# Kernel optimization log

Measured on AMD Instinct MI355X. Metric: run time of the kernel, lower is better.

The kernel has to match this reference:

```python
import jax, jax.numpy as jnp
import numpy as np

N = 32768
NIN = 12
NC = 16
HID = 512
K = 8
B = 3.0
L = 8
D_HALF = NIN // 2                      # 6
DIN = D_HALF + NC                      # conditioner input
DOUT = (3 * K - 1) * (NIN - D_HALF)    # conditioner output
MIN_W = 1e-3
MIN_H = 1e-3
MIN_D = 1e-3
DERIV_CONST = float(np.log(np.exp(1.0 - MIN_D) - 1.0))  # softplus^{-1}(1-min_d)


def setup_inputs() -> dict:
    key = jax.random.key(0)
    ks = jax.random.split(key, 12)
    z = jax.random.normal(ks[0], (N, NIN), dtype=jnp.float32)
    c = jax.random.normal(ks[1], (N, NC), dtype=jnp.float32)

    def lin(k, fan_in, shape):
        bound = 1.0 / np.sqrt(fan_in)
        return jax.random.uniform(k, shape, jnp.float32, -bound, bound)

    W0 = lin(ks[2], DIN, (L, DIN, HID)); b0 = lin(ks[3], DIN, (L, HID))
    W1 = lin(ks[4], HID, (L, HID, HID)); b1 = lin(ks[5], HID, (L, HID))
    W2 = lin(ks[6], HID, (L, HID, HID)); b2 = lin(ks[7], HID, (L, HID))
    W3 = lin(ks[8], HID, (L, HID, DOUT)); b3 = lin(ks[9], HID, (L, DOUT))

    rng = np.random.default_rng(0)
    perms = jnp.asarray(np.stack([rng.permutation(NIN) for _ in range(L - 1)]),
                        dtype=jnp.int32)  # [L-1, NIN]
    return dict(z=z, c=c, W0=W0, b0=b0, W1=W1, b1=b1, W2=W2, b2=b2,
                W3=W3, b3=b3, perms=perms)


def _rqs(x, uw, uh, ud):
    """Unconstrained rational-quadratic spline (forward).
    x: [N, d2]; uw/uh: [N, d2, K]; ud: [N, d2, K+1] (already edge-padded)."""
    widths = jax.nn.softmax(uw, axis=-1)
    widths = MIN_W + (1.0 - MIN_W * K) * widths
    cw = jnp.cumsum(widths, axis=-1)
    cw = jnp.concatenate([jnp.zeros_like(cw[..., :1]), cw], axis=-1)
    cw = 2.0 * B * cw - B
    cw = cw.at[..., 0].set(-B).at[..., -1].set(B)
    w = cw[..., 1:] - cw[..., :-1]

    heights = jax.nn.softmax(uh, axis=-1)
    heights = MIN_H + (1.0 - MIN_H * K) * heights
    ch = jnp.cumsum(heights, axis=-1)
    ch = jnp.concatenate([jnp.zeros_like(ch[..., :1]), ch], axis=-1)
    ch = 2.0 * B * ch - B
    ch = ch.at[..., 0].set(-B).at[..., -1].set(B)
    h = ch[..., 1:] - ch[..., :-1]

    d = MIN_D + jax.nn.softplus(ud)  # [N, d2, K+1]

    xc = jnp.clip(x, -B, B)  # tails are handled by mask below
    # searchsorted: eps added only to the last knot for the search itself
    cw_search = cw.at[..., -1].add(1e-6)
    idx = jnp.clip(jnp.sum((xc[..., None] >= cw_search).astype(jnp.int32),
                           axis=-1) - 1, 0, K - 1)  # [N, d2]

    def g(a):
        return jnp.take_along_axis(a, idx[..., None], axis=-1)[..., 0]

    icw, iw = g(cw), g(w)
    ich, ih = g(ch), g(h)
    idelta = g(h / w)
    id0 = g(d)
    id1 = g(d[..., 1:])

    theta = (xc - icw) / iw
    t1m = theta * (1.0 - theta)
    num = ih * (idelta * theta**2 + id0 * t1m)
    den = idelta + (id0 + id1 - 2.0 * idelta) * t1m
    out = ich + num / den
    dnum = idelta**2 * (id1 * theta**2 + 2.0 * idelta * t1m
                        + id0 * (1.0 - theta)**2)
    lad = jnp.log(dnum) - 2.0 * jnp.log(den)

    inside = (x >= -B) & (x <= B)
    return jnp.where(inside, out, x), jnp.where(inside, lad, 0.0)


def _flow(z, c, W0, b0, W1, b1, W2, b2, W3, b3, perms):
    x = z
    total_ld = jnp.zeros(z.shape[0], dtype=z.dtype)
    for i in range(L):
        x1, x2 = x[:, :D_HALF], x[:, D_HALF:]
        inp = jnp.concatenate([x1, c], axis=-1)
        h0 = jax.nn.elu(inp @ W0[i] + b0[i])
        h1 = jax.nn.elu(h0 @ W1[i] + b1[i])
        h2 = jax.nn.elu(h1 @ W2[i] + b2[i])
        out = (h2 @ W3[i] + b3[i]).reshape(-1, NIN - D_HALF, 3 * K - 1)
        uw, uh, ud = out[..., :K], out[..., K:2 * K], out[..., 2 * K:]
        ud = jnp.pad(ud, ((0, 0), (0, 0), (1, 1)),
                     constant_values=DERIV_CONST)
        x2n, ld = _rqs(x2, uw, uh, ud)
        total_ld = total_ld + jnp.sum(ld, axis=-1)
        x = jnp.concatenate([x1, x2n], axis=-1)
        if i < L - 1:
            x = x[:, perms[i]]
    return x, total_ld


def reference(z, c, W0, b0, W1, b1, W2, b2, W3, b3, perms):
    return _flow(z, c, W0, b0, W1, b1, W2, b2, W3, b3, perms)
```

## Files before the change

### kernel.cpp

```cpp
#include <hip/hip_runtime.h>
#include <hip/hip_fp16.h>

#define NROWS   32768
#define MT      64
#define NTH     512
#define HS      520
#define OS      148
#define BND     3.0f

typedef _Float16 half_t;
typedef __attribute__((ext_vector_type(8))) _Float16 f16x8;
typedef __attribute__((ext_vector_type(4))) _Float16 f16x4;
typedef __attribute__((ext_vector_type(4))) float    f32x4;


__global__ void pack_frag(const float* __restrict__ src, half_t* __restrict__ dst,
                          int K, int Nn, int NT, int KS) {
  int l = blockIdx.z;
  int frag = blockIdx.x * 4 + (threadIdx.x >> 6);
  int lane = threadIdx.x & 63;
  int NF = NT * KS;
  if (frag >= NF) return;
  int nt = frag / KS, ks = frag - nt * KS;
  int n = nt * 16 + (lane & 15);
  int kb = ks * 32 + (lane >> 4) * 8;
  f16x8 v;
#pragma unroll
  for (int e = 0; e < 8; e++) {
    int k = kb + e;
    v[e] = (k < K && n < Nn) ? (half_t)src[((size_t)l * K + k) * Nn + n] : (half_t)0.f;
  }
  *(f16x8*)(dst + ((size_t)l * NF + frag) * 512 + lane * 8) = v;
}

__device__ __forceinline__ float elu_f(float v) {
  return v > 0.f ? v : (__expf(v) - 1.f);
}

__device__ __forceinline__ void gemm_elu(
    const half_t* A, int as, int ksteps,
    const half_t* __restrict__ Wf, int KSW,
    const float* __restrict__ bias,
    half_t* dst,
    int w, int lane, int lm, int lk) {
  f16x8 a[2][4], b[4][2];
#pragma unroll
  for (int half = 0; half < 2; half++) {
    const int ntb = w * 4 + half * 2;
    f32x4 acc[4][2];
#pragma unroll
    for (int i = 0; i < 4; i++)
#pragma unroll
      for (int j = 0; j < 2; j++) acc[i][j] = (f32x4){0.f, 0.f, 0.f, 0.f};

    const bool prefilled = (ksteps == 16) && (half == 1);
    if (!prefilled) {
#pragma unroll
      for (int s = 0; s < 4; s++)
        if (s < ksteps) {
#pragma unroll
          for (int nt = 0; nt < 2; nt++)
            b[s][nt] = *(const f16x8*)(Wf + ((size_t)((ntb + nt) * KSW + s)) * 512 + lane * 8);
        }
#pragma unroll
      for (int s = 0; s < 2; s++)
        if (s < ksteps) {
          int ko = s * 32 + lk * 8;
#pragma unroll
          for (int mf = 0; mf < 4; mf++)
            a[s][mf] = *(const f16x8*)(A + (mf * 16 + lm) * as + ko);
        }
    }
#pragma unroll
    for (int ks = 0; ks < ksteps; ks++) {
      const int sl = ks & 3, asx = ks & 1;
#pragma unroll
      for (int nt = 0; nt < 2; nt++)
#pragma unroll
        for (int mf = 0; mf < 4; mf++)
          acc[mf][nt] = __builtin_amdgcn_mfma_f32_16x16x32_f16(b[sl][nt], a[asx][mf], acc[mf][nt], 0, 0, 0);
      if (ks + 4 < ksteps) {
#pragma unroll
        for (int nt = 0; nt < 2; nt++)
          b[sl][nt] = *(const f16x8*)(Wf + ((size_t)((ntb + nt) * KSW + ks + 4)) * 512 + lane * 8);
      } else if (ksteps == 16 && half == 0) {
#pragma unroll
        for (int nt = 0; nt < 2; nt++)
          b[sl][nt] = *(const f16x8*)(Wf + ((size_t)((ntb + 2 + nt) * KSW + (ks - 12))) * 512 + lane * 8);
      }
      if (ks + 2 < ksteps) {
        int ko = (ks + 2) * 32 + lk * 8;
#pragma unroll
        for (int mf = 0; mf < 4; mf++)
          a[asx][mf] = *(const f16x8*)(A + (mf * 16 + lm) * HS + ko);
      } else if (ksteps == 16 && half == 0) {
        int ko = (ks - 14) * 32 + lk * 8;
#pragma unroll
        for (int mf = 0; mf < 4; mf++)
          a[asx][mf] = *(const f16x8*)(A + (mf * 16 + lm) * HS + ko);
      }
    }
#pragma unroll
    for (int nt = 0; nt < 2; nt++) {
      int n0 = w * 64 + half * 32 + nt * 16 + lk * 4;
      f32x4 bv = *(const f32x4*)(bias + n0);
#pragma unroll
      for (int mf = 0; mf < 4; mf++) {
        f16x4 pv;
#pragma unroll
        for (int r = 0; r < 4; r++) pv[r] = (half_t)elu_f(acc[mf][nt][r] + bv[r]);
        *(f16x4*)(dst + (mf * 16 + lm) * HS + n0) = pv;
      }
    }
  }
}

__device__ __forceinline__ void gemm_out(
    const half_t* A,
    const half_t* __restrict__ Wf,
    const float* __restrict__ bias,
    float* outb,
    int w, int lane, int lm, int lk) {
  f32x4 acc[4][2];
#pragma unroll
  for (int i = 0; i < 4; i++)
#pragma unroll
    for (int j = 0; j < 2; j++) acc[i][j] = (f32x4){0.f, 0.f, 0.f, 0.f};
  const bool has2 = (w == 0);

  f16x8 a[2][4], b[4][2];
#pragma unroll
  for (int s = 0; s < 4; s++) {
    b[s][0] = *(const f16x8*)(Wf + ((size_t)(w * 16 + s)) * 512 + lane * 8);
    if (has2) b[s][1] = *(const f16x8*)(Wf + ((size_t)(8 * 16 + s)) * 512 + lane * 8);
  }
#pragma unroll
  for (int s = 0; s < 2; s++) {
    int ko = s * 32 + lk * 8;
#pragma unroll
    for (int mf = 0; mf < 4; mf++)
      a[s][mf] = *(const f16x8*)(A + (mf * 16 + lm) * HS + ko);
  }
#pragma unroll
  for (int ks = 0; ks < 16; ks++) {
    const int sl = ks & 3, asx = ks & 1;
#pragma unroll
    for (int mf = 0; mf < 4; mf++)
      acc[mf][0] = __builtin_amdgcn_mfma_f32_16x16x32_f16(b[sl][0], a[asx][mf], acc[mf][0], 0, 0, 0);
    if (has2)
#pragma unroll
      for (int mf = 0; mf < 4; mf++)
        acc[mf][1] = __builtin_amdgcn_mfma_f32_16x16x32_f16(b[sl][1], a[asx][mf], acc[mf][1], 0, 0, 0);
    if (ks + 4 < 16) {
      b[sl][0] = *(const f16x8*)(Wf + ((size_t)(w * 16 + ks + 4)) * 512 + lane * 8);
      if (has2) b[sl][1] = *(const f16x8*)(Wf + ((size_t)(128 + ks + 4)) * 512 + lane * 8);
    }
    if (ks + 2 < 16) {
      int ko = (ks + 2) * 32 + lk * 8;
#pragma unroll
      for (int mf = 0; mf < 4; mf++)
        a[asx][mf] = *(const f16x8*)(A + (mf * 16 + lm) * HS + ko);
    }
  }
  {
    int n0 = w * 16 + lk * 4;
    f32x4 bv = *(const f32x4*)(bias + n0);
#pragma unroll
    for (int mf = 0; mf < 4; mf++) {
      f32x4 ov = acc[mf][0] + bv;
      *(f32x4*)(outb + (mf * 16 + lm) * OS + n0) = ov;
    }
  }
  if (has2) {
    int n0 = 128 + lk * 4;
    f32x4 bv;
#pragma unroll
    for (int r = 0; r < 4; r++) bv[r] = (n0 + r < 138) ? bias[n0 + r] : 0.f;
#pragma unroll
    for (int mf = 0; mf < 4; mf++) {
      f32x4 ov = acc[mf][1] + bv;
      *(f32x4*)(outb + (mf * 16 + lm) * OS + n0) = ov;
    }
  }
}

__global__ __launch_bounds__(NTH, 2) __attribute__((amdgpu_waves_per_eu(2, 2)))
void flow_kernel(const float* __restrict__ z, const float* __restrict__ c,
                 const float* __restrict__ b0, const float* __restrict__ b1,
                 const float* __restrict__ b2, const float* __restrict__ b3,
                 const int* __restrict__ perms,
                 const half_t* __restrict__ W0F, const half_t* __restrict__ W1F,
                 const half_t* __restrict__ W2F, const half_t* __restrict__ W3F,
                 float* __restrict__ out) {
  __shared__ half_t hbufA[MT * HS];
  __shared__ __align__(16) char smemB[MT * HS * 2];
  __shared__ half_t inpb[MT * 40];
  __shared__ half_t cbuf[MT * 16];
  __shared__ float xbuf[MT][12];
  __shared__ float ldpart[MT][6];
  __shared__ float ldtot[MT];
  __shared__ int   permbuf[7][12];

  half_t* hbufB  = (half_t*)smemB;
  float*  outbuf = (float*)smemB;

  int tid = threadIdx.x;
  int w = tid >> 6, lane = tid & 63;
  int lm = lane & 15, lk = lane >> 4;
  int row0 = blockIdx.x * MT;

  for (int it = tid; it < MT * 12; it += NTH) xbuf[it / 12][it % 12] = z[(size_t)row0 * 12 + it];
  for (int it = tid; it < MT * 16; it += NTH) cbuf[it] = (half_t)c[(size_t)row0 * 16 + it];
  for (int it = tid; it < 84; it += NTH) permbuf[it / 12][it % 12] = perms[it];
  if (tid < MT) ldtot[tid] = 0.f;
  __syncthreads();

  for (int l = 0; l < 8; l++) {
    for (int it = tid; it < MT * 32; it += NTH) {
      int m = it >> 5, k = it & 31;
      half_t bv;
      if (k < 6)       bv = (half_t)xbuf[m][k];
      else if (k < 22) bv = cbuf[m * 16 + (k - 6)];
      else             bv = (half_t)0.f;
      inpb[m * 40 + k] = bv;
    }
    __syncthreads();
    gemm_elu(inpb, 40, 1,  W0F + (size_t)l * 32 * 512,      1,  b0 + l * 512, hbufA, w, lane, lm, lk);
    __syncthreads();
    gemm_elu(hbufA, HS, 16, W1F + (size_t)l * 512 * 512,   16,  b1 + l * 512, hbufB, w, lane, lm, lk);
    __syncthreads();
    gemm_elu(hbufB, HS, 16, W2F + (size_t)l * 512 * 512,   16,  b2 + l * 512, hbufA, w, lane, lm, lk);
    __syncthreads();
    gemm_out(hbufA, W3F + (size_t)l * 144 * 512, b3 + l * 138, outbuf, w, lane, lm, lk);
    __syncthreads();

    if (tid < MT * 6) {
      int m = tid / 6, j = tid % 6;
      const float* pr = outbuf + m * OS + j * 23;
      float uw[8], uh[8], dd[9];
#pragma unroll
      for (int i = 0; i < 8; i++) uw[i] = pr[i];
#pragma unroll
      for (int i = 0; i < 8; i++) uh[i] = pr[8 + i];
      dd[0] = 1.f; dd[8] = 1.f;
#pragma unroll
      for (int i = 0; i < 7; i++) {
        float u = pr[16 + i];
        float sp = (u > 15.f) ? u : log1pf(__expf(u));
        dd[i + 1] = 0.001f + sp;
      }
      float mw = uw[0];
#pragma unroll
      for (int i = 1; i < 8; i++) mw = fmaxf(mw, uw[i]);
      float ew[8], sw = 0.f;
#pragma unroll
      for (int i = 0; i < 8; i++) { ew[i] = __expf(uw[i] - mw); sw += ew[i]; }
      float invw = 1.f / sw;
      float cw[9]; cw[0] = -BND;
      float a = 0.f;
#pragma unroll
      for (int i = 0; i < 8; i++) { a += 0.001f + 0.992f * ew[i] * invw; cw[i + 1] = 2.f * BND * a - BND; }
      cw[8] = BND;
      float mh = uh[0];
#pragma unroll
      for (int i = 1; i < 8; i++) mh = fmaxf(mh, uh[i]);
      float eh[8], sh = 0.f;
#pragma unroll
      for (int i = 0; i < 8; i++) { eh[i] = __expf(uh[i] - mh); sh += eh[i]; }
      float invh = 1.f / sh;
      float ch[9]; ch[0] = -BND;
      float ah = 0.f;
#pragma unroll
      for (int i = 0; i < 8; i++) { ah += 0.001f + 0.992f * eh[i] * invh; ch[i + 1] = 2.f * BND * ah - BND; }
      ch[8] = BND;

      float x2 = xbuf[m][6 + j];
      float xc = fminf(fmaxf(x2, -BND), BND);
      int cnt = 0;
#pragma unroll
      for (int i = 0; i < 9; i++) {
        float edge = (i == 8) ? (cw[8] + 1e-6f) : cw[i];
        cnt += (xc >= edge) ? 1 : 0;
      }
      int idx = cnt - 1; idx = idx < 0 ? 0 : (idx > 7 ? 7 : idx);
      float icw = cw[0], iw = cw[1] - cw[0], ich = ch[0], ih = ch[1] - ch[0], d0 = dd[0], d1 = dd[1];
#pragma unroll
      for (int i = 0; i < 8; i++) {
        if (idx == i) {
          icw = cw[i]; iw = cw[i + 1] - cw[i];
          ich = ch[i]; ih = ch[i + 1] - ch[i];
          d0 = dd[i]; d1 = dd[i + 1];
        }
      }
      float delta = ih / iw;
      float th  = (xc - icw) / iw;
      float t1m = th * (1.f - th);
      float num = ih * (delta * th * th + d0 * t1m);
      float den = delta + (d0 + d1 - 2.f * delta) * t1m;
      float outv = ich + num / den;
      float dnum = delta * delta * (d1 * th * th + 2.f * delta * t1m + d0 * (1.f - th) * (1.f - th));
      float lad = logf(dnum) - 2.f * logf(den);
      bool inside = (x2 >= -BND) && (x2 <= BND);
      xbuf[m][6 + j] = inside ? outv : x2;
      ldpart[m][j]   = inside ? lad : 0.f;
    }
    __syncthreads();
    if (tid < MT) {
      float s = ldtot[tid];
#pragma unroll
      for (int j = 0; j < 6; j++) s += ldpart[tid][j];
      ldtot[tid] = s;
    }
    if (l < 7) {
      float v0 = xbuf[tid / 12][permbuf[l][tid % 12]];
      float v1 = 0.f;
      int it1 = tid + NTH;
      if (it1 < MT * 12) v1 = xbuf[it1 / 12][permbuf[l][it1 % 12]];
      __syncthreads();
      xbuf[tid / 12][tid % 12] = v0;
      if (it1 < MT * 12) xbuf[it1 / 12][it1 % 12] = v1;
    }
    __syncthreads();
  }

  for (int it = tid; it < MT * 12; it += NTH) out[(size_t)row0 * 12 + it] = xbuf[it / 12][it % 12];
  if (tid < MT) out[(size_t)NROWS * 12 + row0 + tid] = ldtot[tid];
}

extern "C" void kernel_launch(void* const* d_in, const int* in_sizes, int n_in,
                              void* d_out, int out_size, void* d_ws, size_t ws_size,
                              hipStream_t stream) {
  const float* z  = (const float*)d_in[0];
  const float* c  = (const float*)d_in[1];
  const float* W0 = (const float*)d_in[2];
  const float* b0 = (const float*)d_in[3];
  const float* W1 = (const float*)d_in[4];
  const float* b1 = (const float*)d_in[5];
  const float* W2 = (const float*)d_in[6];
  const float* b2 = (const float*)d_in[7];
  const float* W3 = (const float*)d_in[8];
  const float* b3 = (const float*)d_in[9];
  const int* perms = (const int*)d_in[10];

  unsigned short* wsu = (unsigned short*)d_ws;
  half_t* W0F = (half_t*)(wsu + 0);
  half_t* W1F = (half_t*)(wsu + 131072);
  half_t* W2F = (half_t*)(wsu + 2228224);
  half_t* W3F = (half_t*)(wsu + 4325376);

  pack_frag<<<dim3(8,   1, 8), dim3(256), 0, stream>>>(W0, W0F, 22,  512, 32, 1);
  pack_frag<<<dim3(128, 1, 8), dim3(256), 0, stream>>>(W1, W1F, 512, 512, 32, 16);
  pack_frag<<<dim3(128, 1, 8), dim3(256), 0, stream>>>(W2, W2F, 512, 512, 32, 16);
  pack_frag<<<dim3(36,  1, 8), dim3(256), 0, stream>>>(W3, W3F, 512, 138, 9,  16);

  flow_kernel<<<dim3(NROWS / MT), dim3(NTH), 0, stream>>>(
      z, c, b0, b1, b2, b3, perms, W0F, W1F, W2F, W3F, (float*)d_out);
}
```

Measured before the change: 551.7 us.

## Store hidden activations in MFMA fragment-packed shared memory layout

Hidden activation buffers in shared memory are reorganized from padded row-major into the same per-lane fragment order used by the MFMA A operand, so each lane reads a contiguous 16-byte chunk indexed by lane. The ELU epilogue writes results directly into this packed order, and the input staging packs the first layer's operand similarly. This aims to reduce address arithmetic and LDS bank conflicts on operand reads and drops the row padding, at the cost of possibly less favorable store patterns in the epilogue.

```diff
diff --git a/kernel.cpp b/kernel.cpp
--- a/kernel.cpp
+++ b/kernel.cpp
@@ -4,7 +4,6 @@
 #define NROWS   32768
 #define MT      64
 #define NTH     512
-#define HS      520
 #define OS      148
 #define BND     3.0f
 
@@ -38,7 +37,7 @@
 }
 
 __device__ __forceinline__ void gemm_elu(
-    const half_t* A, int as, int ksteps,
+    const half_t* A, int KSA, int ksteps,
     const half_t* __restrict__ Wf, int KSW,
     const float* __restrict__ bias,
     half_t* dst,
@@ -65,10 +64,9 @@
 #pragma unroll
       for (int s = 0; s < 2; s++)
         if (s < ksteps) {
-          int ko = s * 32 + lk * 8;
 #pragma unroll
           for (int mf = 0; mf < 4; mf++)
-            a[s][mf] = *(const f16x8*)(A + (mf * 16 + lm) * as + ko);
+            a[s][mf] = *(const f16x8*)(A + ((size_t)(mf * KSA + s)) * 512 + lane * 8);
         }
     }
 #pragma unroll
@@ -89,27 +87,29 @@
           b[sl][nt] = *(const f16x8*)(Wf + ((size_t)((ntb + 2 + nt) * KSW + (ks - 12))) * 512 + lane * 8);
       }
       if (ks + 2 < ksteps) {
-        int ko = (ks + 2) * 32 + lk * 8;
 #pragma unroll
         for (int mf = 0; mf < 4; mf++)
-          a[asx][mf] = *(const f16x8*)(A + (mf * 16 + lm) * HS + ko);
+          a[asx][mf] = *(const f16x8*)(A + ((size_t)(mf * KSA + ks + 2)) * 512 + lane * 8);
       } else if (ksteps == 16 && half == 0) {
-        int ko = (ks - 14) * 32 + lk * 8;
 #pragma unroll
         for (int mf = 0; mf < 4; mf++)
-          a[asx][mf] = *(const f16x8*)(A + (mf * 16 + lm) * HS + ko);
-      }
-    }
-#pragma unroll
-    for (int nt = 0; nt < 2; nt++) {
-      int n0 = w * 64 + half * 32 + nt * 16 + lk * 4;
-      f32x4 bv = *(const f32x4*)(bias + n0);
-#pragma unroll
-      for (int mf = 0; mf < 4; mf++) {
-        f16x4 pv;
-#pragma unroll
-        for (int r = 0; r < 4; r++) pv[r] = (half_t)elu_f(acc[mf][nt][r] + bv[r]);
-        *(f16x4*)(dst + (mf * 16 + lm) * HS + n0) = pv;
+          a[asx][mf] = *(const f16x8*)(A + ((size_t)(mf * KSA + (ks - 14))) * 512 + lane * 8);
+      }
+    }
+    {
+      const int ksg = w * 2 + half;
+#pragma unroll
+      for (int nt = 0; nt < 2; nt++) {
+        int n0 = w * 64 + half * 32 + nt * 16 + lk * 4;
+        f32x4 bv = *(const f32x4*)(bias + n0);
+        int lane_dst = (nt * 2 + (lk >> 1)) * 16 + lm;
+#pragma unroll
+        for (int mf = 0; mf < 4; mf++) {
+          f16x4 pv;
+#pragma unroll
+          for (int r = 0; r < 4; r++) pv[r] = (half_t)elu_f(acc[mf][nt][r] + bv[r]);
+          *(f16x4*)(dst + ((size_t)(mf * 16 + ksg)) * 512 + lane_dst * 8 + (lk & 1) * 4) = pv;
+        }
       }
     }
   }
@@ -136,10 +136,9 @@
   }
 #pragma unroll
   for (int s = 0; s < 2; s++) {
-    int ko = s * 32 + lk * 8;
 #pragma unroll
     for (int mf = 0; mf < 4; mf++)
-      a[s][mf] = *(const f16x8*)(A + (mf * 16 + lm) * HS + ko);
+      a[s][mf] = *(const f16x8*)(A + ((size_t)(mf * 16 + s)) * 512 + lane * 8);
   }
 #pragma unroll
   for (int ks = 0; ks < 16; ks++) {
@@ -156,10 +155,9 @@
       if (has2) b[sl][1] = *(const f16x8*)(Wf + ((size_t)(128 + ks + 4)) * 512 + lane * 8);
     }
     if (ks + 2 < 16) {
-      int ko = (ks + 2) * 32 + lk * 8;
 #pragma unroll
       for (int mf = 0; mf < 4; mf++)
-        a[asx][mf] = *(const f16x8*)(A + (mf * 16 + lm) * HS + ko);
+        a[asx][mf] = *(const f16x8*)(A + ((size_t)(mf * 16 + ks + 2)) * 512 + lane * 8);
     }
   }
   {
@@ -192,9 +190,9 @@
                  const half_t* __restrict__ W0F, const half_t* __restrict__ W1F,
                  const half_t* __restrict__ W2F, const half_t* __restrict__ W3F,
                  float* __restrict__ out) {
-  __shared__ half_t hbufA[MT * HS];
-  __shared__ __align__(16) char smemB[MT * HS * 2];
-  __shared__ half_t inpb[MT * 40];
+  __shared__ half_t hbufA[4 * 16 * 512];
+  __shared__ __align__(16) char smemB[4 * 16 * 512 * 2];
+  __shared__ half_t inpb[4 * 512];
   __shared__ half_t cbuf[MT * 16];
   __shared__ float xbuf[MT][12];
   __shared__ float ldpart[MT][6];
@@ -222,14 +220,14 @@
       if (k < 6)       bv = (half_t)xbuf[m][k];
       else if (k < 22) bv = cbuf[m * 16 + (k - 6)];
       else             bv = (half_t)0.f;
-      inpb[m * 40 + k] = bv;
-    }
-    __syncthreads();
-    gemm_elu(inpb, 40, 1,  W0F + (size_t)l * 32 * 512,      1,  b0 + l * 512, hbufA, w, lane, lm, lk);
-    __syncthreads();
-    gemm_elu(hbufA, HS, 16, W1F + (size_t)l * 512 * 512,   16,  b1 + l * 512, hbufB, w, lane, lm, lk);
-    __syncthreads();
-    gemm_elu(hbufB, HS, 16, W2F + (size_t)l * 512 * 512,   16,  b2 + l * 512, hbufA, w, lane, lm, lk);
+      inpb[(m >> 4) * 512 + ((k >> 3) * 16 + (m & 15)) * 8 + (k & 7)] = bv;
+    }
+    __syncthreads();
+    gemm_elu(inpb, 1, 1,   W0F + (size_t)l * 32 * 512,     1,  b0 + l * 512, hbufA, w, lane, lm, lk);
+    __syncthreads();
+    gemm_elu(hbufA, 16, 16, W1F + (size_t)l * 512 * 512,  16,  b1 + l * 512, hbufB, w, lane, lm, lk);
+    __syncthreads();
+    gemm_elu(hbufB, 16, 16, W2F + (size_t)l * 512 * 512,  16,  b2 + l * 512, hbufA, w, lane, lm, lk);
     __syncthreads();
     gemm_out(hbufA, W3F + (size_t)l * 144 * 512, b3 + l * 138, outbuf, w, lane, lm, lk);
     __syncthreads();
```

New measurement: 502.4 us. 1.1x faster.
